# Optimization experiments

Hardware: AMD Instinct MI355X
Metric: run time of the kernel (lower is better)

## Reference

```python
import jax, jax.numpy as jnp
import numpy as np

B, L, E, H, D = 32, 512, 256, 8, 64
SCALE = int(D ** 0.5)  # matches TF: int(hidden_dim ** 0.5) == 8


def setup_inputs() -> dict:
    key = jax.random.key(0)
    ks = jax.random.split(key, 6)
    return {
        "x": jax.random.normal(ks[0], (B, L, E), dtype=jnp.float32),
        "positional": jax.random.normal(ks[1], (L, E), dtype=jnp.float32) * 0.02,
        "Wq": jax.random.normal(ks[2], (H, E, D), dtype=jnp.float32) * 0.05,
        "Wk": jax.random.normal(ks[3], (H, E, D), dtype=jnp.float32) * 0.05,
        "Wv": jax.random.normal(ks[4], (H, E, D), dtype=jnp.float32) * 0.05,
        "Wo": jax.random.normal(ks[5], (H * D, E), dtype=jnp.float32) * 0.05,
    }


def reference(x, positional, Wq, Wk, Wv, Wo):
    act = jnp.tanh  # activation='tanh'
    xp = x + positional                                   # [B,L,E]
    # Batched per-head projections with activation applied post-matmul
    q = act(jnp.einsum('ble,hed->bhld', xp, Wq))          # [B,H,L,D]
    k = act(jnp.einsum('ble,hed->bhld', xp, Wk))
    v = act(jnp.einsum('ble,hed->bhld', xp, Wv))
    score = jnp.einsum('bhqd,bhkd->bhqk', q, k) / SCALE   # [B,H,L,L]
    attn = jax.nn.softmax(score, axis=-1)
    out = jnp.einsum('bhqk,bhkd->bhqd', attn, v)          # [B,H,L,D]
    # concat heads along last axis (head-major) -> [B,L,H*D]
    out = jnp.transpose(out, (0, 2, 1, 3)).reshape(B, L, H * D)
    return jnp.einsum('blf,fe->ble', out, Wo) + act(xp)   # [B,L,E]
```

## Files before the change

### kernel.cpp

```cpp
#include <hip/hip_runtime.h>
#include <cstdint>

#define NB 32
#define NL 512
#define NE 256
#define NH 8
#define ND 64
#define NM 16384
#define NHD 512

using half8  = __attribute__((ext_vector_type(8))) _Float16;
using half4  = __attribute__((ext_vector_type(4))) _Float16;
using f32x4  = __attribute__((ext_vector_type(4))) float;
using f32x16 = __attribute__((ext_vector_type(16))) float;
using u32x2  = __attribute__((ext_vector_type(2))) unsigned int;

__device__ __forceinline__ f32x4 mfma16(half8 a, half8 b, f32x4 c) {
    return __builtin_amdgcn_mfma_f32_16x16x32_f16(a, b, c, 0, 0, 0);
}
__device__ __forceinline__ f32x16 mfma32(half8 a, half8 b, f32x16 c) {
    return __builtin_amdgcn_mfma_f32_32x32x16_f16(a, b, c, 0, 0, 0);
}
__device__ __forceinline__ void cp16_g2l(const void* g, void* l) {
    __builtin_amdgcn_global_load_lds(
        (const __attribute__((address_space(1))) void*)g,
        (__attribute__((address_space(3))) void*)l, 16, 0, 0);
}
__device__ __forceinline__ float exp2fast(float x) {
    return __builtin_amdgcn_exp2f(x);
}
__device__ __forceinline__ float fast_tanh(float x) {
    float xc = fminf(fmaxf(x, -9.f), 9.f);
    float t = exp2fast(xc * 2.88539008178f);
    return (t - 1.f) * __builtin_amdgcn_rcpf(t + 1.f);
}
__device__ __forceinline__ uint32_t pk16(float a, float b) {
    auto h2 = __builtin_amdgcn_cvt_pkrtz(a, b);
    return __builtin_bit_cast(uint32_t, h2);
}

__global__ __launch_bounds__(256) void prep(
        const float* __restrict__ x, const float* __restrict__ pos,
        const float* __restrict__ Wq, const float* __restrict__ Wk,
        const float* __restrict__ Wv, const float* __restrict__ Wo,
        _Float16* __restrict__ wqkv, _Float16* __restrict__ woh,
        _Float16* __restrict__ xph) {
    int bid = blockIdx.x;
    if (bid < 2048) {
        int idx = bid * 256 + threadIdx.x;
        if (idx < 1536 * 256) {
            int n = idx >> 8, e = idx & 255;
            int s = n >> 9, h = (n >> 6) & 7, d = n & 63;
            const float* W = (s == 0) ? Wq : (s == 1) ? Wk : Wv;
            wqkv[idx] = (_Float16)W[(h * NE + e) * ND + d];
        } else {
            int j = idx - 1536 * 256;
            int e = j >> 9, f = j & 511;
            woh[j] = (_Float16)Wo[f * NE + e];
        }
    } else {
        int i = ((bid - 2048) * 256 + threadIdx.x) * 4;
        float4 xv = *(const float4*)(x + i);
        float4 pv = *(const float4*)(pos + (i & (NL * NE - 1)));
        half4 o;
        o[0] = (_Float16)(xv.x + pv.x);
        o[1] = (_Float16)(xv.y + pv.y);
        o[2] = (_Float16)(xv.z + pv.z);
        o[3] = (_Float16)(xv.w + pv.w);
        *(half4*)(xph + i) = o;
    }
}

__global__ __launch_bounds__(512, 2) void attn_fused(
        const _Float16* __restrict__ wqkv, const _Float16* __restrict__ xph,
        _Float16* __restrict__ attn_out) {
    __shared__ _Float16 Kp[512 * 64];
    __shared__ _Float16 Vtp[64 * 512];
    _Float16* Xs = Kp;
    _Float16* Ws = Kp + 128 * 64;
    _Float16* Qs = Vtp;

    int tid = threadIdx.x;
    int w8 = tid >> 6, l = tid & 63;
    int l31 = l & 31, hi = l >> 5;
    int rt = w8 & 3, d2w = w8 >> 2;
    int g0 = ((blockIdx.x & 7) << 5) + (blockIdx.x >> 3);
    int h = g0 & 7, b = g0 >> 3;
    const float C1 = 0.125f * 1.44269504089f;
    const float C4 = 4.f * 1.44269504089f;

    int lrow8 = l >> 3;
    int kc16 = (l & 7) ^ lrow8;
    const _Float16* xg = xph + (size_t)(b * NL) * 256;
    const _Float16* wg = wqkv + (size_t)(h * 64) * 256;

    f32x16 acc_q[4] = {}, acc_k[4] = {}, acc_v[4] = {};
    for (int kt2 = 0; kt2 < 4; ++kt2) {
#pragma unroll
        for (int r = 0; r < 4; ++r) {
#pragma unroll
            for (int i = 0; i < 2; ++i) {
                int c = w8 * 2 + i;
                int row = c * 8 + lrow8;
                cp16_g2l(xg + (size_t)(r * 128 + row) * 256 + kt2 * 64 + kc16 * 8,
                         Xs + c * 512);
            }
            if (r == 0) {
                int row = w8 * 8 + lrow8;
#pragma unroll
                for (int s = 0; s < 3; ++s)
                    cp16_g2l(wg + (size_t)s * 512 * 256 + (size_t)row * 256 + kt2 * 64 + kc16 * 8,
                             Ws + s * 4096 + w8 * 512);
            }
            __syncthreads();
#pragma unroll
            for (int ks2 = 0; ks2 < 4; ++ks2) {
                int rowb = rt * 32 + l31;
                half8 bf = *(const half8*)(Xs + rowb * 64 + (((ks2 * 2 + hi) ^ (rowb & 7)) << 3));
                int rowa = d2w * 32 + l31;
                int sa = rowa * 64 + (((ks2 * 2 + hi) ^ (rowa & 7)) << 3);
                half8 aq = *(const half8*)(Ws + sa);
                half8 ak = *(const half8*)(Ws + 4096 + sa);
                half8 av = *(const half8*)(Ws + 8192 + sa);
                acc_q[r] = mfma32(aq, bf, acc_q[r]);
                acc_k[r] = mfma32(ak, bf, acc_k[r]);
                acc_v[r] = mfma32(bf, av, acc_v[r]);
            }
            __syncthreads();
        }
    }

#pragma unroll
    for (int r = 0; r < 4; ++r) {
        uint32_t cq[4][2], ck[4][2];
#pragma unroll
        for (int a = 0; a < 4; ++a)
#pragma unroll
            for (int p = 0; p < 2; ++p) {
                cq[a][p] = pk16(fast_tanh(acc_q[r][4 * a + 2 * p]),
                                fast_tanh(acc_q[r][4 * a + 2 * p + 1]));
                ck[a][p] = pk16(fast_tanh(acc_k[r][4 * a + 2 * p]),
                                fast_tanh(acc_k[r][4 * a + 2 * p + 1]));
            }
        int rowq = r * 128 + rt * 32 + l31;
#pragma unroll
        for (int ks = 0; ks < 2; ++ks) {
            u32x2 q0 = __builtin_amdgcn_permlane32_swap(cq[2 * ks][0], cq[2 * ks + 1][0], false, false);
            u32x2 q1 = __builtin_amdgcn_permlane32_swap(cq[2 * ks][1], cq[2 * ks + 1][1], false, false);
            u32x2 k0 = __builtin_amdgcn_permlane32_swap(ck[2 * ks][0], ck[2 * ks + 1][0], false, false);
            u32x2 k1 = __builtin_amdgcn_permlane32_swap(ck[2 * ks][1], ck[2 * ks + 1][1], false, false);
            union { uint32_t u[4]; half8 h8; } pq, pk;
            pq.u[0] = q0[0]; pq.u[1] = q1[0]; pq.u[2] = q0[1]; pq.u[3] = q1[1];
            pk.u[0] = k0[0]; pk.u[1] = k1[0]; pk.u[2] = k0[1]; pk.u[3] = k1[1];
            int uu = d2w * 4 + ks * 2 + hi;
            *(half8*)(Qs + rowq * 64 + ((uu ^ (rowq & 7)) << 3)) = pq.h8;
            *(half8*)(Kp + rowq * 64 + ((uu ^ (rowq & 7)) << 3)) = pk.h8;
        }
    }
    __syncthreads();
    half8 qf[2][4];
#pragma unroll
    for (int qs = 0; qs < 2; ++qs)
#pragma unroll
        for (int ks = 0; ks < 4; ++ks) {
            int q = w8 * 64 + qs * 32 + l31;
            qf[qs][ks] = *(const half8*)(Qs + q * 64 + (((ks * 2 + hi) ^ (q & 7)) << 3));
        }
    __syncthreads();
#pragma unroll
    for (int r = 0; r < 4; ++r) {
        uint32_t cv[4][2];
#pragma unroll
        for (int a = 0; a < 4; ++a)
#pragma unroll
            for (int p = 0; p < 2; ++p)
                cv[a][p] = pk16(fast_tanh(acc_v[r][4 * a + 2 * p]),
                                fast_tanh(acc_v[r][4 * a + 2 * p + 1]));
        int d = d2w * 32 + l31;
#pragma unroll
        for (int ks = 0; ks < 2; ++ks) {
            u32x2 v0 = __builtin_amdgcn_permlane32_swap(cv[2 * ks][0], cv[2 * ks + 1][0], false, false);
            u32x2 v1 = __builtin_amdgcn_permlane32_swap(cv[2 * ks][1], cv[2 * ks + 1][1], false, false);
            union { uint32_t u[4]; half8 h8; } pv;
            pv.u[0] = v0[0]; pv.u[1] = v1[0]; pv.u[2] = v0[1]; pv.u[3] = v1[1];
            int uu = r * 16 + rt * 4 + ks * 2 + hi;
            *(half8*)(Vtp + d * 512 + ((uu ^ (d & 7)) << 3)) = pv.h8;
        }
    }
    __syncthreads();

    f32x16 acc_o[2][2] = {};
    float lrow[2] = {0.f, 0.f};
    for (int kt = 0; kt < 8; ++kt) {
#pragma unroll
        for (int qs = 0; qs < 2; ++qs) {
            f32x16 acc_s[2] = {};
            __builtin_amdgcn_s_setprio(1);
#pragma unroll
            for (int ks = 0; ks < 4; ++ks)
#pragma unroll
                for (int kb2 = 0; kb2 < 2; ++kb2) {
                    int key = kt * 64 + kb2 * 32 + l31;
                    half8 kb = *(const half8*)(Kp + key * 64 + (((ks * 2 + hi) ^ (key & 7)) << 3));
                    acc_s[kb2] = mfma32(kb, qf[qs][ks], acc_s[kb2]);
                }
            __builtin_amdgcn_s_setprio(0);
            float rs = 0.f;
            uint32_t cw[2][4][2];
#pragma unroll
            for (int kb2 = 0; kb2 < 2; ++kb2)
#pragma unroll
                for (int a = 0; a < 4; ++a)
#pragma unroll
                    for (int p = 0; p < 2; ++p) {
                        float p0 = exp2fast(fmaf(acc_s[kb2][4 * a + 2 * p],     C1, -C4));
                        float p1 = exp2fast(fmaf(acc_s[kb2][4 * a + 2 * p + 1], C1, -C4));
                        rs += p0 + p1;
                        cw[kb2][a][p] = pk16(p0, p1);
                    }
            lrow[qs] += rs;
            __builtin_amdgcn_s_setprio(1);
#pragma unroll
            for (int ks = 0; ks < 4; ++ks) {
                int kb2 = ks >> 1, s = ks & 1;
                u32x2 r0 = __builtin_amdgcn_permlane32_swap(
                    cw[kb2][2 * s][0], cw[kb2][2 * s + 1][0], false, false);
                u32x2 r1 = __builtin_amdgcn_permlane32_swap(
                    cw[kb2][2 * s][1], cw[kb2][2 * s + 1][1], false, false);
                union { uint32_t u[4]; half8 h8; } pu;
                pu.u[0] = r0[0]; pu.u[1] = r1[0]; pu.u[2] = r0[1]; pu.u[3] = r1[1];
#pragma unroll
                for (int d2 = 0; d2 < 2; ++d2) {
                    int d = d2 * 32 + l31;
                    int uu = kt * 8 + ks * 2 + hi;
                    half8 vb = *(const half8*)(Vtp + d * 512 + ((uu ^ (d & 7)) << 3));
                    acc_o[qs][d2] = mfma32(pu.h8, vb, acc_o[qs][d2]);
                }
            }
            __builtin_amdgcn_s_setprio(0);
        }
    }
#pragma unroll
    for (int qs = 0; qs < 2; ++qs) {
        lrow[qs] += __shfl_xor(lrow[qs], 32);
        size_t orow0 = (size_t)(b * NL + w8 * 64 + qs * 32);
#pragma unroll
        for (int c = 0; c < 4; ++c)
#pragma unroll
            for (int r = 0; r < 4; ++r) {
                int qrow = c * 8 + hi * 4 + r;
                float inv = 1.f / __shfl(lrow[qs], qrow);
#pragma unroll
                for (int d2 = 0; d2 < 2; ++d2)
                    attn_out[(orow0 + qrow) * NHD + h * ND + d2 * 32 + l31] =
                        (_Float16)(acc_o[qs][d2][c * 4 + r] * inv);
            }
    }
}

__global__ __launch_bounds__(256) void final_gemm(
        const _Float16* __restrict__ woh, const _Float16* __restrict__ attn,
        const _Float16* __restrict__ xph, float* __restrict__ out) {
    __shared__ _Float16 Alds[2][128 * 64];
    __shared__ _Float16 Blds[2][64 * 64];
    int tid = threadIdx.x;
    int w = tid >> 6, l = tid & 63;
    int bid = blockIdx.x;
    int xcd = bid & 7, local = bid >> 3;
    int tn = local & 1;
    int tm = xcd * 32 + (local >> 1);
    int wn = w >> 1, wm = w & 1;
    int m16 = l & 15, g = l >> 4;
    int lrow8 = l >> 3;
    int kc16 = (l & 7) ^ lrow8;
    f32x4 acc[4][2] = {};

    const _Float16* Ag = woh + (size_t)tn * 128 * 512;
    const _Float16* Bg = attn + (size_t)tm * 64 * 512;

#define FIN_STAGE(kt, buf)                                                    \
    _Pragma("unroll") for (int i = 0; i < 4; ++i) {                           \
        int cA = w * 4 + i;                                                   \
        int row = cA * 8 + lrow8;                                             \
        cp16_g2l(Ag + (size_t)row * 512 + (kt) * 64 + kc16 * 8,               \
                 &Alds[buf][cA * 512]);                                       \
    }                                                                         \
    _Pragma("unroll") for (int i = 0; i < 2; ++i) {                           \
        int cB = w * 2 + i;                                                   \
        int row = cB * 8 + lrow8;                                             \
        cp16_g2l(Bg + (size_t)row * 512 + (kt) * 64 + kc16 * 8,               \
                 &Blds[buf][cB * 512]);                                       \
    }

    FIN_STAGE(0, 0);
    __syncthreads();
    int cur = 0;
    for (int kt = 0; kt < 8; ++kt) {
        if (kt < 7) { FIN_STAGE(kt + 1, cur ^ 1); }
#pragma unroll
        for (int ks = 0; ks < 2; ++ks) {
            half8 af[4], bf[2];
#pragma unroll
            for (int f = 0; f < 4; ++f) {
                int ra = wn * 64 + f * 16 + m16;
                af[f] = *(const half8*)(&Alds[cur][ra * 64 + (((ks * 4 + g) ^ (ra & 7)) << 3)]);
            }
#pragma unroll
            for (int f = 0; f < 2; ++f) {
                int rb = wm * 32 + f * 16 + m16;
                bf[f] = *(const half8*)(&Blds[cur][rb * 64 + (((ks * 4 + g) ^ (rb & 7)) << 3)]);
            }
#pragma unroll
            for (int nf = 0; nf < 4; ++nf)
#pragma unroll
                for (int mf = 0; mf < 2; ++mf)
                    acc[nf][mf] = mfma16(af[nf], bf[mf], acc[nf][mf]);
        }
        __syncthreads();
        cur ^= 1;
    }
#undef FIN_STAGE
#pragma unroll
    for (int nf = 0; nf < 4; ++nf) {
        int e = tn * 128 + wn * 64 + nf * 16 + g * 4;
#pragma unroll
        for (int mf = 0; mf < 2; ++mf) {
            int m = tm * 64 + wm * 32 + mf * 16 + m16;
            half4 hx = *(const half4*)(xph + (size_t)m * NE + e);
            f32x4 v = acc[nf][mf];
            float4 o;
            o.x = v[0] + fast_tanh((float)hx[0]);
            o.y = v[1] + fast_tanh((float)hx[1]);
            o.z = v[2] + fast_tanh((float)hx[2]);
            o.w = v[3] + fast_tanh((float)hx[3]);
            *(float4*)(out + (size_t)m * NE + e) = o;
        }
    }
}

extern "C" void kernel_launch(void* const* d_in, const int* in_sizes, int n_in,
                              void* d_out, int out_size, void* d_ws, size_t ws_size,
                              hipStream_t stream) {
    const float* x   = (const float*)d_in[0];
    const float* pos = (const float*)d_in[1];
    const float* Wq  = (const float*)d_in[2];
    const float* Wk  = (const float*)d_in[3];
    const float* Wv  = (const float*)d_in[4];
    const float* Wo  = (const float*)d_in[5];
    float* out = (float*)d_out;

    char* ws = (char*)d_ws;
    _Float16* xph   = (_Float16*)(ws);
    _Float16* wqkv  = (_Float16*)(ws + 8388608);
    _Float16* woh   = (_Float16*)(ws + 9175040);
    _Float16* attn  = (_Float16*)(ws + 9437184);

    prep<<<dim3(6144), dim3(256), 0, stream>>>(x, pos, Wq, Wk, Wv, Wo, wqkv, woh, xph);
    attn_fused<<<dim3(256), dim3(512), 0, stream>>>(wqkv, xph, attn);
    final_gemm<<<dim3(512), dim3(256), 0, stream>>>(woh, attn, xph, out);
}
```

Before: 72.25 us.

## Use 1024-thread attention blocks with split QK and V projection phases

The fused attention kernel now launches 16 waves per block instead of 8, so each wave handles 32 query rows. The QKV projection is split into a Q/K pass (Q kept in registers, K written to LDS) and a separate V pass, with a new small LDS buffer for weight tiles. The goal is to cut per-wave accumulator register pressure and add more waves to hide latency across the 256 blocks. The cost is that X tiles are loaded from global memory twice, and occupancy drops to one block per CU with more barriers.

```diff
diff --git a/kernel.cpp b/kernel.cpp
--- a/kernel.cpp
+++ b/kernel.cpp
@@ -71,19 +71,17 @@
     }
 }
 
-__global__ __launch_bounds__(512, 2) void attn_fused(
+__global__ __launch_bounds__(1024, 1) void attn_fused(
         const _Float16* __restrict__ wqkv, const _Float16* __restrict__ xph,
         _Float16* __restrict__ attn_out) {
     __shared__ _Float16 Kp[512 * 64];
     __shared__ _Float16 Vtp[64 * 512];
-    _Float16* Xs = Kp;
-    _Float16* Ws = Kp + 128 * 64;
-    _Float16* Qs = Vtp;
+    __shared__ _Float16 Wst[2 * 64 * 64];
+    _Float16* Xs = Vtp;
 
     int tid = threadIdx.x;
-    int w8 = tid >> 6, l = tid & 63;
+    int w = tid >> 6, l = tid & 63;
     int l31 = l & 31, hi = l >> 5;
-    int rt = w8 & 3, d2w = w8 >> 2;
     int g0 = ((blockIdx.x & 7) << 5) + (blockIdx.x >> 3);
     int h = g0 & 7, b = g0 >> 3;
     const float C1 = 0.125f * 1.44269504089f;
@@ -92,170 +90,192 @@
     int lrow8 = l >> 3;
     int kc16 = (l & 7) ^ lrow8;
     const _Float16* xg = xph + (size_t)(b * NL) * 256;
-    const _Float16* wg = wqkv + (size_t)(h * 64) * 256;
-
-    f32x16 acc_q[4] = {}, acc_k[4] = {}, acc_v[4] = {};
+    const _Float16* wgq = wqkv + (size_t)(h * 64) * 256;
+    const _Float16* wgk = wgq + (size_t)512 * 256;
+    const _Float16* wgv = wgq + (size_t)1024 * 256;
+
+    f32x16 acc_q[2] = {}, acc_k[2] = {};
     for (int kt2 = 0; kt2 < 4; ++kt2) {
 #pragma unroll
-        for (int r = 0; r < 4; ++r) {
-#pragma unroll
-            for (int i = 0; i < 2; ++i) {
-                int c = w8 * 2 + i;
-                int row = c * 8 + lrow8;
-                cp16_g2l(xg + (size_t)(r * 128 + row) * 256 + kt2 * 64 + kc16 * 8,
-                         Xs + c * 512);
-            }
-            if (r == 0) {
-                int row = w8 * 8 + lrow8;
-#pragma unroll
-                for (int s = 0; s < 3; ++s)
-                    cp16_g2l(wg + (size_t)s * 512 * 256 + (size_t)row * 256 + kt2 * 64 + kc16 * 8,
-                             Ws + s * 4096 + w8 * 512);
-            }
-            __syncthreads();
-#pragma unroll
-            for (int ks2 = 0; ks2 < 4; ++ks2) {
-                int rowb = rt * 32 + l31;
-                half8 bf = *(const half8*)(Xs + rowb * 64 + (((ks2 * 2 + hi) ^ (rowb & 7)) << 3));
-                int rowa = d2w * 32 + l31;
-                int sa = rowa * 64 + (((ks2 * 2 + hi) ^ (rowa & 7)) << 3);
-                half8 aq = *(const half8*)(Ws + sa);
-                half8 ak = *(const half8*)(Ws + 4096 + sa);
-                half8 av = *(const half8*)(Ws + 8192 + sa);
-                acc_q[r] = mfma32(aq, bf, acc_q[r]);
-                acc_k[r] = mfma32(ak, bf, acc_k[r]);
-                acc_v[r] = mfma32(bf, av, acc_v[r]);
-            }
-            __syncthreads();
-        }
-    }
-
-#pragma unroll
-    for (int r = 0; r < 4; ++r) {
-        uint32_t cq[4][2], ck[4][2];
-#pragma unroll
-        for (int a = 0; a < 4; ++a)
-#pragma unroll
-            for (int p = 0; p < 2; ++p) {
-                cq[a][p] = pk16(fast_tanh(acc_q[r][4 * a + 2 * p]),
-                                fast_tanh(acc_q[r][4 * a + 2 * p + 1]));
-                ck[a][p] = pk16(fast_tanh(acc_k[r][4 * a + 2 * p]),
-                                fast_tanh(acc_k[r][4 * a + 2 * p + 1]));
-            }
-        int rowq = r * 128 + rt * 32 + l31;
-#pragma unroll
-        for (int ks = 0; ks < 2; ++ks) {
-            u32x2 q0 = __builtin_amdgcn_permlane32_swap(cq[2 * ks][0], cq[2 * ks + 1][0], false, false);
-            u32x2 q1 = __builtin_amdgcn_permlane32_swap(cq[2 * ks][1], cq[2 * ks + 1][1], false, false);
-            u32x2 k0 = __builtin_amdgcn_permlane32_swap(ck[2 * ks][0], ck[2 * ks + 1][0], false, false);
-            u32x2 k1 = __builtin_amdgcn_permlane32_swap(ck[2 * ks][1], ck[2 * ks + 1][1], false, false);
+        for (int j = 0; j < 4; ++j) {
+            int c = j * 16 + w;
+            cp16_g2l(xg + (size_t)(c * 8 + lrow8) * 256 + kt2 * 64 + kc16 * 8,
+                     Xs + c * 512);
+        }
+        {
+            const _Float16* ws = (w < 8) ? wgq : wgk;
+            int row = (w & 7) * 8 + lrow8;
+            cp16_g2l(ws + (size_t)row * 256 + kt2 * 64 + kc16 * 8, Wst + w * 512);
+        }
+        __syncthreads();
+        int rowb = w * 32 + l31;
+#pragma unroll
+        for (int ks2 = 0; ks2 < 4; ++ks2) {
+            int u = ks2 * 2 + hi;
+            half8 bf = *(const half8*)(Xs + rowb * 64 + ((u ^ (rowb & 7)) << 3));
+#pragma unroll
+            for (int d2 = 0; d2 < 2; ++d2) {
+                int ra = d2 * 32 + l31;
+                int sa = ra * 64 + ((u ^ (ra & 7)) << 3);
+                half8 aq = *(const half8*)(Wst + sa);
+                half8 ak = *(const half8*)(Wst + 4096 + sa);
+                acc_q[d2] = mfma32(aq, bf, acc_q[d2]);
+                acc_k[d2] = mfma32(ak, bf, acc_k[d2]);
+            }
+        }
+        __syncthreads();
+    }
+    half8 qf[4];
+    {
+        uint32_t cq[2][4][2], ck[2][4][2];
+#pragma unroll
+        for (int d2 = 0; d2 < 2; ++d2)
+#pragma unroll
+            for (int a = 0; a < 4; ++a)
+#pragma unroll
+                for (int p = 0; p < 2; ++p) {
+                    cq[d2][a][p] = pk16(fast_tanh(acc_q[d2][4 * a + 2 * p]),
+                                        fast_tanh(acc_q[d2][4 * a + 2 * p + 1]));
+                    ck[d2][a][p] = pk16(fast_tanh(acc_k[d2][4 * a + 2 * p]),
+                                        fast_tanh(acc_k[d2][4 * a + 2 * p + 1]));
+                }
+        int row = w * 32 + l31;
+#pragma unroll
+        for (int ks = 0; ks < 4; ++ks) {
+            int d2 = ks >> 1, s = ks & 1;
+            u32x2 q0 = __builtin_amdgcn_permlane32_swap(
+                cq[d2][2 * s][0], cq[d2][2 * s + 1][0], false, false);
+            u32x2 q1 = __builtin_amdgcn_permlane32_swap(
+                cq[d2][2 * s][1], cq[d2][2 * s + 1][1], false, false);
+            u32x2 k0 = __builtin_amdgcn_permlane32_swap(
+                ck[d2][2 * s][0], ck[d2][2 * s + 1][0], false, false);
+            u32x2 k1 = __builtin_amdgcn_permlane32_swap(
+                ck[d2][2 * s][1], ck[d2][2 * s + 1][1], false, false);
             union { uint32_t u[4]; half8 h8; } pq, pk;
             pq.u[0] = q0[0]; pq.u[1] = q1[0]; pq.u[2] = q0[1]; pq.u[3] = q1[1];
             pk.u[0] = k0[0]; pk.u[1] = k1[0]; pk.u[2] = k0[1]; pk.u[3] = k1[1];
-            int uu = d2w * 4 + ks * 2 + hi;
-            *(half8*)(Qs + rowq * 64 + ((uu ^ (rowq & 7)) << 3)) = pq.h8;
-            *(half8*)(Kp + rowq * 64 + ((uu ^ (rowq & 7)) << 3)) = pk.h8;
+            qf[ks] = pq.h8;
+            int uu = ks * 2 + hi;
+            *(half8*)(Kp + row * 64 + ((uu ^ (row & 7)) << 3)) = pk.h8;
         }
     }
     __syncthreads();
-    half8 qf[2][4];
-#pragma unroll
-    for (int qs = 0; qs < 2; ++qs)
+
+    f32x16 acc_v[2] = {};
+    int kb = w >> 1, d2w = w & 1;
+    for (int kt2 = 0; kt2 < 4; ++kt2) {
+#pragma unroll
+        for (int j = 0; j < 4; ++j) {
+            int c = j * 16 + w;
+            cp16_g2l(xg + (size_t)(c * 8 + lrow8) * 256 + kt2 * 64 + kc16 * 8,
+                     Xs + c * 512);
+        }
+        if (w < 8) {
+            int row = w * 8 + lrow8;
+            cp16_g2l(wgv + (size_t)row * 256 + kt2 * 64 + kc16 * 8, Wst + w * 512);
+        }
+        __syncthreads();
+#pragma unroll
+        for (int ks2 = 0; ks2 < 4; ++ks2) {
+            int u = ks2 * 2 + hi;
+            int rw = d2w * 32 + l31;
+            half8 wv = *(const half8*)(Wst + rw * 64 + ((u ^ (rw & 7)) << 3));
+#pragma unroll
+            for (int kb2 = 0; kb2 < 2; ++kb2) {
+                int rx = kb * 64 + kb2 * 32 + l31;
+                half8 xa = *(const half8*)(Xs + rx * 64 + ((u ^ (rx & 7)) << 3));
+                acc_v[kb2] = mfma32(xa, wv, acc_v[kb2]);
+            }
+        }
+        __syncthreads();
+    }
+    {
+        uint32_t cv[2][4][2];
+#pragma unroll
+        for (int kb2 = 0; kb2 < 2; ++kb2)
+#pragma unroll
+            for (int a = 0; a < 4; ++a)
+#pragma unroll
+                for (int p = 0; p < 2; ++p)
+                    cv[kb2][a][p] = pk16(fast_tanh(acc_v[kb2][4 * a + 2 * p]),
+                                         fast_tanh(acc_v[kb2][4 * a + 2 * p + 1]));
+        int d = d2w * 32 + l31;
 #pragma unroll
         for (int ks = 0; ks < 4; ++ks) {
-            int q = w8 * 64 + qs * 32 + l31;
-            qf[qs][ks] = *(const half8*)(Qs + q * 64 + (((ks * 2 + hi) ^ (q & 7)) << 3));
-        }
-    __syncthreads();
-#pragma unroll
-    for (int r = 0; r < 4; ++r) {
-        uint32_t cv[4][2];
-#pragma unroll
-        for (int a = 0; a < 4; ++a)
-#pragma unroll
-            for (int p = 0; p < 2; ++p)
-                cv[a][p] = pk16(fast_tanh(acc_v[r][4 * a + 2 * p]),
-                                fast_tanh(acc_v[r][4 * a + 2 * p + 1]));
-        int d = d2w * 32 + l31;
-#pragma unroll
-        for (int ks = 0; ks < 2; ++ks) {
-            u32x2 v0 = __builtin_amdgcn_permlane32_swap(cv[2 * ks][0], cv[2 * ks + 1][0], false, false);
-            u32x2 v1 = __builtin_amdgcn_permlane32_swap(cv[2 * ks][1], cv[2 * ks + 1][1], false, false);
+            int kb2 = ks >> 1, s = ks & 1;
+            u32x2 v0 = __builtin_amdgcn_permlane32_swap(
+                cv[kb2][2 * s][0], cv[kb2][2 * s + 1][0], false, false);
+            u32x2 v1 = __builtin_amdgcn_permlane32_swap(
+                cv[kb2][2 * s][1], cv[kb2][2 * s + 1][1], false, false);
             union { uint32_t u[4]; half8 h8; } pv;
             pv.u[0] = v0[0]; pv.u[1] = v1[0]; pv.u[2] = v0[1]; pv.u[3] = v1[1];
-            int uu = r * 16 + rt * 4 + ks * 2 + hi;
-            *(half8*)(Vtp + d * 512 + ((uu ^ (d & 7)) << 3)) = pv.h8;
+            int guu = kb * 8 + kb2 * 4 + s * 2 + hi;
+            *(half8*)(Vtp + d * 512 + ((guu ^ (d & 7)) << 3)) = pv.h8;
         }
     }
     __syncthreads();
 
-    f32x16 acc_o[2][2] = {};
-    float lrow[2] = {0.f, 0.f};
+    f32x16 acc_o[2] = {};
+    float lrow = 0.f;
     for (int kt = 0; kt < 8; ++kt) {
-#pragma unroll
-        for (int qs = 0; qs < 2; ++qs) {
-            f32x16 acc_s[2] = {};
-            __builtin_amdgcn_s_setprio(1);
-#pragma unroll
-            for (int ks = 0; ks < 4; ++ks)
-#pragma unroll
-                for (int kb2 = 0; kb2 < 2; ++kb2) {
-                    int key = kt * 64 + kb2 * 32 + l31;
-                    half8 kb = *(const half8*)(Kp + key * 64 + (((ks * 2 + hi) ^ (key & 7)) << 3));
-                    acc_s[kb2] = mfma32(kb, qf[qs][ks], acc_s[kb2]);
+        f32x16 acc_s[2] = {};
+        __builtin_amdgcn_s_setprio(1);
+#pragma unroll
+        for (int ks = 0; ks < 4; ++ks)
+#pragma unroll
+            for (int kb2 = 0; kb2 < 2; ++kb2) {
+                int key = kt * 64 + kb2 * 32 + l31;
+                half8 kbf = *(const half8*)(Kp + key * 64 + (((ks * 2 + hi) ^ (key & 7)) << 3));
+                acc_s[kb2] = mfma32(kbf, qf[ks], acc_s[kb2]);
+            }
+        __builtin_amdgcn_s_setprio(0);
+        float rs = 0.f;
+        uint32_t cw[2][4][2];
+#pragma unroll
+        for (int kb2 = 0; kb2 < 2; ++kb2)
+#pragma unroll
+            for (int a = 0; a < 4; ++a)
+#pragma unroll
+                for (int p = 0; p < 2; ++p) {
+                    float p0 = exp2fast(fmaf(acc_s[kb2][4 * a + 2 * p],     C1, -C4));
+                    float p1 = exp2fast(fmaf(acc_s[kb2][4 * a + 2 * p + 1], C1, -C4));
+                    rs += p0 + p1;
+                    cw[kb2][a][p] = pk16(p0, p1);
                 }
-            __builtin_amdgcn_s_setprio(0);
-            float rs = 0.f;
-            uint32_t cw[2][4][2];
-#pragma unroll
-            for (int kb2 = 0; kb2 < 2; ++kb2)
-#pragma unroll
-                for (int a = 0; a < 4; ++a)
-#pragma unroll
-                    for (int p = 0; p < 2; ++p) {
-                        float p0 = exp2fast(fmaf(acc_s[kb2][4 * a + 2 * p],     C1, -C4));
-                        float p1 = exp2fast(fmaf(acc_s[kb2][4 * a + 2 * p + 1], C1, -C4));
-                        rs += p0 + p1;
-                        cw[kb2][a][p] = pk16(p0, p1);
-                    }
-            lrow[qs] += rs;
-            __builtin_amdgcn_s_setprio(1);
-#pragma unroll
-            for (int ks = 0; ks < 4; ++ks) {
-                int kb2 = ks >> 1, s = ks & 1;
-                u32x2 r0 = __builtin_amdgcn_permlane32_swap(
-                    cw[kb2][2 * s][0], cw[kb2][2 * s + 1][0], false, false);
-                u32x2 r1 = __builtin_amdgcn_permlane32_swap(
-                    cw[kb2][2 * s][1], cw[kb2][2 * s + 1][1], false, false);
-                union { uint32_t u[4]; half8 h8; } pu;
-                pu.u[0] = r0[0]; pu.u[1] = r1[0]; pu.u[2] = r0[1]; pu.u[3] = r1[1];
-#pragma unroll
-                for (int d2 = 0; d2 < 2; ++d2) {
-                    int d = d2 * 32 + l31;
-                    int uu = kt * 8 + ks * 2 + hi;
-                    half8 vb = *(const half8*)(Vtp + d * 512 + ((uu ^ (d & 7)) << 3));
-                    acc_o[qs][d2] = mfma32(pu.h8, vb, acc_o[qs][d2]);
-                }
-            }
-            __builtin_amdgcn_s_setprio(0);
-        }
-    }
-#pragma unroll
-    for (int qs = 0; qs < 2; ++qs) {
-        lrow[qs] += __shfl_xor(lrow[qs], 32);
-        size_t orow0 = (size_t)(b * NL + w8 * 64 + qs * 32);
-#pragma unroll
-        for (int c = 0; c < 4; ++c)
-#pragma unroll
-            for (int r = 0; r < 4; ++r) {
-                int qrow = c * 8 + hi * 4 + r;
-                float inv = 1.f / __shfl(lrow[qs], qrow);
-#pragma unroll
-                for (int d2 = 0; d2 < 2; ++d2)
-                    attn_out[(orow0 + qrow) * NHD + h * ND + d2 * 32 + l31] =
-                        (_Float16)(acc_o[qs][d2][c * 4 + r] * inv);
-            }
-    }
+        lrow += rs;
+        __builtin_amdgcn_s_setprio(1);
+#pragma unroll
+        for (int ks = 0; ks < 4; ++ks) {
+            int kb2 = ks >> 1, s = ks & 1;
+            u32x2 r0 = __builtin_amdgcn_permlane32_swap(
+                cw[kb2][2 * s][0], cw[kb2][2 * s + 1][0], false, false);
+            u32x2 r1 = __builtin_amdgcn_permlane32_swap(
+                cw[kb2][2 * s][1], cw[kb2][2 * s + 1][1], false, false);
+            union { uint32_t u[4]; half8 h8; } pu;
+            pu.u[0] = r0[0]; pu.u[1] = r1[0]; pu.u[2] = r0[1]; pu.u[3] = r1[1];
+#pragma unroll
+            for (int d2 = 0; d2 < 2; ++d2) {
+                int d = d2 * 32 + l31;
+                int uu = kt * 8 + ks * 2 + hi;
+                half8 vb = *(const half8*)(Vtp + d * 512 + ((uu ^ (d & 7)) << 3));
+                acc_o[d2] = mfma32(pu.h8, vb, acc_o[d2]);
+            }
+        }
+        __builtin_amdgcn_s_setprio(0);
+    }
+    lrow += __shfl_xor(lrow, 32);
+    size_t orow0 = (size_t)(b * NL + w * 32);
+#pragma unroll
+    for (int c = 0; c < 4; ++c)
+#pragma unroll
+        for (int r = 0; r < 4; ++r) {
+            int qrow = c * 8 + hi * 4 + r;
+            float inv = 1.f / __shfl(lrow, qrow);
+#pragma unroll
+            for (int d2 = 0; d2 < 2; ++d2)
+                attn_out[(orow0 + qrow) * NHD + h * ND + d2 * 32 + l31] =
+                    (_Float16)(acc_o[d2][c * 4 + r] * inv);
+        }
 }
 
 __global__ __launch_bounds__(256) void final_gemm(
@@ -356,6 +376,6 @@
     _Float16* attn  = (_Float16*)(ws + 9437184);
 
     prep<<<dim3(6144), dim3(256), 0, stream>>>(x, pos, Wq, Wk, Wv, Wo, wqkv, woh, xph);
-    attn_fused<<<dim3(256), dim3(512), 0, stream>>>(wqkv, xph, attn);
+    attn_fused<<<dim3(256), dim3(1024), 0, stream>>>(wqkv, xph, attn);
     final_gemm<<<dim3(512), dim3(256), 0, stream>>>(woh, attn, xph, out);
 }
```

Result: slower. 74.53 us (+3.2%).

## Swap qs/kt loop order and interleave exp with PV MFMA per k-slice

Applied to the files above, without the earlier changes.

Moves the query-subtile loop outside the key-tile loop, so each pass keeps only one pair of output accumulators live instead of two. The exp/pack work is also split per 16-key slice and placed right before the matching PV MFMAs, so VALU work can overlap with matrix work and the packed probability buffer shrinks. The intent is to cut register pressure and improve overlap. The cost is that the K and V LDS reads are repeated for each query subtile rather than shared across both.

```diff
diff --git a/kernel.cpp b/kernel.cpp
--- a/kernel.cpp
+++ b/kernel.cpp
@@ -189,11 +189,11 @@
     }
     __syncthreads();
 
-    f32x16 acc_o[2][2] = {};
-    float lrow[2] = {0.f, 0.f};
-    for (int kt = 0; kt < 8; ++kt) {
-#pragma unroll
-        for (int qs = 0; qs < 2; ++qs) {
+#pragma unroll
+    for (int qs = 0; qs < 2; ++qs) {
+        f32x16 acc_o[2] = {};
+        float lrow = 0.f;
+        for (int kt = 0; kt < 8; ++kt) {
             f32x16 acc_s[2] = {};
             __builtin_amdgcn_s_setprio(1);
 #pragma unroll
@@ -206,54 +206,48 @@
                 }
             __builtin_amdgcn_s_setprio(0);
             float rs = 0.f;
-            uint32_t cw[2][4][2];
-#pragma unroll
-            for (int kb2 = 0; kb2 < 2; ++kb2)
-#pragma unroll
-                for (int a = 0; a < 4; ++a)
-#pragma unroll
-                    for (int p = 0; p < 2; ++p) {
-                        float p0 = exp2fast(fmaf(acc_s[kb2][4 * a + 2 * p],     C1, -C4));
-                        float p1 = exp2fast(fmaf(acc_s[kb2][4 * a + 2 * p + 1], C1, -C4));
-                        rs += p0 + p1;
-                        cw[kb2][a][p] = pk16(p0, p1);
-                    }
-            lrow[qs] += rs;
-            __builtin_amdgcn_s_setprio(1);
 #pragma unroll
             for (int ks = 0; ks < 4; ++ks) {
                 int kb2 = ks >> 1, s = ks & 1;
-                u32x2 r0 = __builtin_amdgcn_permlane32_swap(
-                    cw[kb2][2 * s][0], cw[kb2][2 * s + 1][0], false, false);
-                u32x2 r1 = __builtin_amdgcn_permlane32_swap(
-                    cw[kb2][2 * s][1], cw[kb2][2 * s + 1][1], false, false);
+                float p0 = exp2fast(fmaf(acc_s[kb2][8 * s + 0], C1, -C4));
+                float p1 = exp2fast(fmaf(acc_s[kb2][8 * s + 1], C1, -C4));
+                float p2 = exp2fast(fmaf(acc_s[kb2][8 * s + 2], C1, -C4));
+                float p3 = exp2fast(fmaf(acc_s[kb2][8 * s + 3], C1, -C4));
+                float p4 = exp2fast(fmaf(acc_s[kb2][8 * s + 4], C1, -C4));
+                float p5 = exp2fast(fmaf(acc_s[kb2][8 * s + 5], C1, -C4));
+                float p6 = exp2fast(fmaf(acc_s[kb2][8 * s + 6], C1, -C4));
+                float p7 = exp2fast(fmaf(acc_s[kb2][8 * s + 7], C1, -C4));
+                rs += ((p0 + p1) + (p2 + p3)) + ((p4 + p5) + (p6 + p7));
+                uint32_t we0 = pk16(p0, p1), we1 = pk16(p2, p3);
+                uint32_t wo0 = pk16(p4, p5), wo1 = pk16(p6, p7);
+                u32x2 r0 = __builtin_amdgcn_permlane32_swap(we0, wo0, false, false);
+                u32x2 r1 = __builtin_amdgcn_permlane32_swap(we1, wo1, false, false);
                 union { uint32_t u[4]; half8 h8; } pu;
                 pu.u[0] = r0[0]; pu.u[1] = r1[0]; pu.u[2] = r0[1]; pu.u[3] = r1[1];
+                __builtin_amdgcn_s_setprio(1);
 #pragma unroll
                 for (int d2 = 0; d2 < 2; ++d2) {
                     int d = d2 * 32 + l31;
                     int uu = kt * 8 + ks * 2 + hi;
                     half8 vb = *(const half8*)(Vtp + d * 512 + ((uu ^ (d & 7)) << 3));
-                    acc_o[qs][d2] = mfma32(pu.h8, vb, acc_o[qs][d2]);
+                    acc_o[d2] = mfma32(pu.h8, vb, acc_o[d2]);
                 }
-            }
-            __builtin_amdgcn_s_setprio(0);
-        }
-    }
-#pragma unroll
-    for (int qs = 0; qs < 2; ++qs) {
-        lrow[qs] += __shfl_xor(lrow[qs], 32);
+                __builtin_amdgcn_s_setprio(0);
+            }
+            lrow += rs;
+        }
+        lrow += __shfl_xor(lrow, 32);
         size_t orow0 = (size_t)(b * NL + w8 * 64 + qs * 32);
 #pragma unroll
         for (int c = 0; c < 4; ++c)
 #pragma unroll
             for (int r = 0; r < 4; ++r) {
                 int qrow = c * 8 + hi * 4 + r;
-                float inv = 1.f / __shfl(lrow[qs], qrow);
+                float inv = 1.f / __shfl(lrow, qrow);
 #pragma unroll
                 for (int d2 = 0; d2 < 2; ++d2)
                     attn_out[(orow0 + qrow) * NHD + h * ND + d2 * 32 + l31] =
-                        (_Float16)(acc_o[qs][d2][c * 4 + r] * inv);
+                        (_Float16)(acc_o[d2][c * 4 + r] * inv);
             }
     }
 }
```

Result: no change. 73.21 us (+1.3%).

## Double-buffer X tiles in QKV projection loop to overlap loads with MFMA

Applied to the files above, without the earlier changes.

Restructures the fused QKV projection loop into a flat 16-step software pipeline. The next X tile is prefetched asynchronously into an alternate LDS buffer while MFMAs run on the current one. Weight tiles are reloaded after the trailing barrier of each kt2 group, and explicit vmcnt waits plus scheduling barriers replace the paired __syncthreads. This is meant to hide global-to-LDS latency behind compute. In exchange it uses more LDS region and relies on precise waitcnt ordering, where a wrong count would be a correctness hazard.

```diff
diff --git a/kernel.cpp b/kernel.cpp
--- a/kernel.cpp
+++ b/kernel.cpp
@@ -76,8 +76,7 @@
         _Float16* __restrict__ attn_out) {
     __shared__ _Float16 Kp[512 * 64];
     __shared__ _Float16 Vtp[64 * 512];
-    _Float16* Xs = Kp;
-    _Float16* Ws = Kp + 128 * 64;
+    _Float16* Ws = Kp + 16384;
     _Float16* Qs = Vtp;
 
     int tid = threadIdx.x;
@@ -95,40 +94,64 @@
     const _Float16* wg = wqkv + (size_t)(h * 64) * 256;
 
     f32x16 acc_q[4] = {}, acc_k[4] = {}, acc_v[4] = {};
-    for (int kt2 = 0; kt2 < 4; ++kt2) {
-#pragma unroll
-        for (int r = 0; r < 4; ++r) {
-#pragma unroll
-            for (int i = 0; i < 2; ++i) {
-                int c = w8 * 2 + i;
-                int row = c * 8 + lrow8;
-                cp16_g2l(xg + (size_t)(r * 128 + row) * 256 + kt2 * 64 + kc16 * 8,
-                         Xs + c * 512);
-            }
-            if (r == 0) {
-                int row = w8 * 8 + lrow8;
-#pragma unroll
-                for (int s = 0; s < 3; ++s)
-                    cp16_g2l(wg + (size_t)s * 512 * 256 + (size_t)row * 256 + kt2 * 64 + kc16 * 8,
-                             Ws + s * 4096 + w8 * 512);
-            }
-            __syncthreads();
-#pragma unroll
-            for (int ks2 = 0; ks2 < 4; ++ks2) {
-                int rowb = rt * 32 + l31;
-                half8 bf = *(const half8*)(Xs + rowb * 64 + (((ks2 * 2 + hi) ^ (rowb & 7)) << 3));
-                int rowa = d2w * 32 + l31;
-                int sa = rowa * 64 + (((ks2 * 2 + hi) ^ (rowa & 7)) << 3);
-                half8 aq = *(const half8*)(Ws + sa);
-                half8 ak = *(const half8*)(Ws + 4096 + sa);
-                half8 av = *(const half8*)(Ws + 8192 + sa);
-                acc_q[r] = mfma32(aq, bf, acc_q[r]);
-                acc_k[r] = mfma32(ak, bf, acc_k[r]);
-                acc_v[r] = mfma32(bf, av, acc_v[r]);
-            }
-            __syncthreads();
-        }
-    }
+
+#define ISSUE_X(kt2_, r_, buf_)                                               \
+    _Pragma("unroll") for (int i = 0; i < 2; ++i) {                           \
+        int c = w8 * 2 + i;                                                   \
+        int row = c * 8 + lrow8;                                              \
+        cp16_g2l(xg + (size_t)((r_) * 128 + row) * 256 + (kt2_) * 64 + kc16 * 8, \
+                 Kp + (buf_) * 8192 + c * 512);                               \
+    }
+#define ISSUE_W(kt2_)                                                         \
+    {                                                                         \
+        int row = w8 * 8 + lrow8;                                             \
+        _Pragma("unroll") for (int s = 0; s < 3; ++s)                         \
+            cp16_g2l(wg + (size_t)s * 512 * 256 + (size_t)row * 256 + (kt2_) * 64 + kc16 * 8, \
+                     Ws + s * 4096 + w8 * 512);                               \
+    }
+#define PA_MFMA(buf_, r_)                                                     \
+    _Pragma("unroll") for (int ks2 = 0; ks2 < 4; ++ks2) {                     \
+        int rowb = rt * 32 + l31;                                             \
+        half8 bf = *(const half8*)(Kp + (buf_) * 8192 + rowb * 64 +           \
+                                   (((ks2 * 2 + hi) ^ (rowb & 7)) << 3));     \
+        int rowa = d2w * 32 + l31;                                            \
+        int sa = rowa * 64 + (((ks2 * 2 + hi) ^ (rowa & 7)) << 3);            \
+        half8 aq = *(const half8*)(Ws + sa);                                  \
+        half8 ak = *(const half8*)(Ws + 4096 + sa);                           \
+        half8 av = *(const half8*)(Ws + 8192 + sa);                           \
+        acc_q[r_] = mfma32(aq, bf, acc_q[r_]);                                \
+        acc_k[r_] = mfma32(ak, bf, acc_k[r_]);                                \
+        acc_v[r_] = mfma32(bf, av, acc_v[r_]);                                \
+    }
+
+    ISSUE_X(0, 0, 0);
+    ISSUE_W(0);
+    asm volatile("s_waitcnt vmcnt(0)" ::: "memory");
+    __builtin_amdgcn_s_barrier();
+    __builtin_amdgcn_sched_barrier(0);
+#pragma unroll
+    for (int it = 0; it < 16; ++it) {
+        int kt2 = it >> 2, r = it & 3, buf = it & 1;
+        if (it < 15) {
+            int nx = it + 1;
+            ISSUE_X(nx >> 2, nx & 3, buf ^ 1);
+            asm volatile("s_waitcnt vmcnt(2)" ::: "memory");
+        } else {
+            asm volatile("s_waitcnt vmcnt(0)" ::: "memory");
+        }
+        __builtin_amdgcn_s_barrier();
+        __builtin_amdgcn_sched_barrier(0);
+        PA_MFMA(buf, r);
+        if (it < 15) {
+            __builtin_amdgcn_sched_barrier(0);
+            __builtin_amdgcn_s_barrier();
+            if (r == 3) ISSUE_W(kt2 + 1);
+        }
+    }
+    __syncthreads();
+#undef ISSUE_X
+#undef ISSUE_W
+#undef PA_MFMA
 
 #pragma unroll
     for (int r = 0; r < 4; ++r) {
```

Result: faster. 69.75 us (median of 2 runs) (-3.5%).
